# Kernel optimization log

Hardware: AMD Instinct MI355X
Metric: run time of the kernel (lower is better)

Reference implementation:

```python
import jax, jax.numpy as jnp
import numpy as np

T = 8  # num_temp_tokens (init arg)
K = 3  # routing conv kernel size (hardcoded in module)


def setup_inputs() -> dict:
    key = jax.random.key(0)
    ks = jax.random.split(key, 7)
    C, CO, NE = 384, 1152, 4
    BT, N = 256, 197
    s = 0.02
    return {
        "x": jax.random.normal(ks[0], (BT, N, C), dtype=jnp.float32),
        "rf_w": jax.random.normal(ks[1], (NE, C), dtype=jnp.float32) * s,
        "rf_b": jax.random.normal(ks[2], (NE,), dtype=jnp.float32) * s,
        "moe_w": jax.random.normal(ks[3], (NE, CO, C, K), dtype=jnp.float32) * s,
        "moe_b": jax.random.normal(ks[4], (NE, CO), dtype=jnp.float32) * s,
        "weight": jax.random.normal(ks[5], (CO, C), dtype=jnp.float32) * s,
        "bias": jax.random.normal(ks[6], (CO,), dtype=jnp.float32) * s,
    }


def _routing(cls, rf_w, rf_b, moe_w, moe_b):
    # cls: (b, C, T). route_func_linear_cls_token_moe forward.
    pooled = cls.mean(axis=2)                       # global avg pool over T -> (b, C)
    rf = pooled @ rf_w.T + rf_b                     # 1x1 conv -> (b, num_experts)
    w = jnp.einsum('be,eock->bock', rf, moe_w)      # per-sample mixed weights (b, 3C, C, K)
    br = rf @ moe_b                                 # per-sample mixed bias (b, 3C)
    clsp = jnp.pad(cls, ((0, 0), (0, 0), (K // 2, K // 2)))
    # sliding windows over T: (b, C, T, K)
    clsw = jnp.stack([clsp[:, :, k:k + cls.shape[2]] for k in range(K)], axis=-1)
    routing = jnp.einsum('bock,bctk->bot', w, clsw) + br[:, :, None] + 1.0  # (b, 3C, T)
    return routing


def reference(x, rf_w, rf_b, moe_w, moe_b, weight, bias):
    bt, n, C = x.shape
    b = bt // T
    xb = x.reshape(b, T, n, C)                      # '(b t) n c -> b t n c'
    cls = xb[:, :, 0, :].transpose(0, 2, 1)         # (b, C, T) cls token stream
    routing = _routing(cls, rf_w, rf_b, moe_w, moe_b)  # (b, 3C, T)
    r = routing.transpose(0, 2, 1)                  # (b, T, 3C)
    rq, rk, rv = jnp.split(r, 3, axis=-1)           # each (b, T, C)
    Wq, Wk, Wv = jnp.split(weight, 3, axis=0)       # each (C, C)
    bq, bk, bv = jnp.split(bias, 3)                 # each (C,)

    def branch(rr, Wc, bc):
        # grouped 1x1 conv with per-(b,t) cin-scaled weight:
        # out[b,t,o,n] = sum_c Wc[o,c] * rr[b,t,c] * x[b,t,n,c] + bc[o]*rr[b,t,o]
        xs = xb * rr[:, :, None, :]                 # (b, T, n, C)
        return jnp.einsum('btnc,oc->bton', xs, Wc) + (bc[None, None, :] * rr)[..., None]

    oq = branch(rq, Wq, bq)
    ok = branch(rk, Wk, bk)
    ov = branch(rv, Wv, bv)
    out = jnp.concatenate([oq, ok, ov], axis=2)     # (b, T, 3C, n)
    return out.reshape(bt, 3 * C, n)
```

## Files before the change

kernel.cpp:

```cpp
#include <hip/hip_runtime.h>
#include <hip/hip_bf16.h>

typedef __attribute__((ext_vector_type(8))) short short8;
typedef __attribute__((ext_vector_type(4))) short short4v;
typedef __attribute__((ext_vector_type(4))) float f32x4;

__device__ __forceinline__ short f2bf(float f) {
    union { float f; unsigned u; } v; v.f = f;
    unsigned r = v.u + 0x7FFF + ((v.u >> 16) & 1);
    return (short)(r >> 16);
}

__device__ __forceinline__ void gll16(const short* g, short* l) {
    __builtin_amdgcn_global_load_lds(
        (const __attribute__((address_space(1))) void*)g,
        (__attribute__((address_space(3))) void*)l, 16, 0, 0);
}

#define NE 4
#define CC 384
#define CO 1152
#define TT 8
#define NN 197
#define NPAD 224
#define NB 32
#define BT 256
#define MOEW_ELEMS 5308416
#define W_ELEMS    442368

__global__ __launch_bounds__(256) void prep_kernel(
    const float* __restrict__ x, const float* __restrict__ rf_w,
    const float* __restrict__ rf_b, const float* __restrict__ moe_w,
    const float* __restrict__ weight,
    short* __restrict__ moeWb, short* __restrict__ Wb,
    short* __restrict__ Yb, float* __restrict__ rf)
{
    int blk = blockIdx.x, tid = threadIdx.x;
    if (blk < NB) {
        __shared__ float clsL[TT * CC];
        __shared__ float pooled[CC];
        int b = blk;
        for (int flat = tid; flat < TT * CC; flat += 256) {
            int t = flat / CC, c = flat - t * CC;
            clsL[flat] = x[(size_t)(b * TT + t) * NN * CC + c];
        }
        __syncthreads();
        for (int c = tid; c < CC; c += 256) {
            float s = 0.f;
            #pragma unroll
            for (int t = 0; t < TT; t++) s += clsL[t * CC + c];
            pooled[c] = s * 0.125f;
        }
        for (int t = 0; t < TT; t++)
            for (int flat = tid; flat < CC * 3; flat += 256) {
                int c = flat / 3, k = flat - c * 3;
                int u = t + k - 1;
                float v = (u >= 0 && u < TT) ? clsL[u * CC + c] : 0.f;
                Yb[(size_t)(b * TT + t) * (CC * 3) + flat] = f2bf(v);
            }
        __syncthreads();
        int wave = tid >> 6, lane = tid & 63;
        float p = 0.f;
        for (int c = lane; c < CC; c += 64) p += pooled[c] * rf_w[wave * CC + c];
        #pragma unroll
        for (int off = 32; off; off >>= 1) p += __shfl_down(p, off, 64);
        if (lane == 0) rf[b * NE + wave] = p + rf_b[wave];
    } else {
        const long NU = (MOEW_ELEMS + W_ELEMS) / 4;
        long step = (long)(gridDim.x - NB) * 256;
        for (long unit = (long)(blk - NB) * 256 + tid; unit < NU; unit += step) {
            long idx = unit * 4;
            float4 v; short* dst;
            if (idx < MOEW_ELEMS) { v = *(const float4*)(moe_w + idx); dst = moeWb + idx; }
            else { long j = idx - MOEW_ELEMS; v = *(const float4*)(weight + j); dst = Wb + j; }
            short4v s;
            s.x = f2bf(v.x); s.y = f2bf(v.y); s.z = f2bf(v.z); s.w = f2bf(v.w);
            *(short4v*)dst = s;
        }
    }
}

__global__ __launch_bounds__(256) void gemm_P(
    const short* __restrict__ A, const short* __restrict__ B, float* __restrict__ P)
{
    __shared__ short A_lds[64 * 64];
    __shared__ short B_lds[64 * 64];
    int bm = blockIdx.x, bn = blockIdx.y, tid = threadIdx.x;
    int wave = tid >> 6, lane = tid & 63, l15 = lane & 15, lq = lane >> 4;
    f32x4 acc[4];
    #pragma unroll
    for (int j = 0; j < 4; j++) acc[j] = (f32x4){0.f, 0.f, 0.f, 0.f};

    for (int kk = 0; kk < 1152 / 64; kk++) {
        __syncthreads();
        #pragma unroll
        for (int j2 = 0; j2 < 2; j2++) {
            int flat = j2 * 256 + tid;
            int row = flat >> 3, seg = flat & 7;
            gll16(A + (size_t)(bm * 64 + row) * 1152 + kk * 64 + seg * 8, &A_lds[flat * 8]);
            gll16(B + (size_t)(bn * 64 + row) * 1152 + kk * 64 + seg * 8, &B_lds[flat * 8]);
        }
        __syncthreads();
        #pragma unroll
        for (int ks = 0; ks < 2; ks++) {
            short8 a = *(short8*)&A_lds[(wave * 16 + l15) * 64 + ks * 32 + lq * 8];
            #pragma unroll
            for (int j = 0; j < 4; j++) {
                short8 bfr = *(short8*)&B_lds[(j * 16 + l15) * 64 + ks * 32 + lq * 8];
                acc[j] = __builtin_amdgcn_mfma_f32_16x16x32_bf16(a, bfr, acc[j], 0, 0, 0);
            }
        }
    }
    #pragma unroll
    for (int j = 0; j < 4; j++)
        #pragma unroll
        for (int reg = 0; reg < 4; reg++) {
            int row = bm * 64 + wave * 16 + lq * 4 + reg;
            int col = bn * 64 + j * 16 + l15;
            P[(size_t)row * 256 + col] = acc[j][reg];
        }
}

__global__ __launch_bounds__(256) void combine_kernel(
    const float* __restrict__ P, const float* __restrict__ rf,
    const float* __restrict__ moe_b, float* __restrict__ r_ws)
{
    __shared__ float rf_l[NB * NE];
    int o = blockIdx.x, tid = threadIdx.x;
    if (tid < NB * NE) rf_l[tid] = rf[tid];
    __syncthreads();
    int b = tid >> 3;
    float acc = 1.0f;
    #pragma unroll
    for (int e = 0; e < NE; e++)
        acc += rf_l[b * NE + e] * (P[(size_t)(e * CO + o) * 256 + tid] + moe_b[e * CO + o]);
    r_ws[(size_t)tid * CO + o] = acc;
}

__global__ __launch_bounds__(256) void xs_scale(
    const float* __restrict__ x, const float* __restrict__ r_ws,
    short* __restrict__ xs)
{
    __shared__ float r_l[CO];
    int bt = blockIdx.x, ng = blockIdx.y, tid = threadIdx.x;
    for (int i = tid; i < CO; i += 256) r_l[i] = r_ws[(size_t)bt * CO + i];
    __syncthreads();
    #pragma unroll
    for (int it = 0; it < 6; it++) {
        int idx = it * 256 + tid;
        int row = idx / 96, cu = idx - row * 96;
        int n = ng * 16 + row;
        float4 v = {0.f, 0.f, 0.f, 0.f};
        if (n < NN) v = *(const float4*)(x + ((size_t)bt * NN + n) * CC + cu * 4);
        #pragma unroll
        for (int br = 0; br < 3; br++) {
            const float* rp = &r_l[br * CC + cu * 4];
            short4v s;
            s.x = f2bf(v.x * rp[0]);
            s.y = f2bf(v.y * rp[1]);
            s.z = f2bf(v.z * rp[2]);
            s.w = f2bf(v.w * rp[3]);
            *(short4v*)(xs + ((size_t)(bt * 3 + br) * NPAD + n) * CC + cu * 4) = s;
        }
    }
}

__global__ __launch_bounds__(256) void main_gemm(
    const short* __restrict__ xs, const short* __restrict__ Wb,
    const float* __restrict__ r_ws, const float* __restrict__ bias,
    float* __restrict__ out)
{
    __shared__ short A_lds[128 * 64];
    __shared__ short B_lds[112 * 64];

    int g = blockIdx.x;
    int u = g & 7, w2 = g >> 3;
    int mt = w2 % 9;
    int pq = u + 8 * (w2 / 9);
    int bt = pq >> 1, nt = pq & 1;
    int tid = threadIdx.x;
    int br = mt / 3;

    const short* Abase = Wb + (size_t)(mt * 128) * CC;
    const short* Bbase = xs + ((size_t)(bt * 3 + br) * NPAD + nt * 112) * CC;

    f32x4 acc[2][7];
    #pragma unroll
    for (int i = 0; i < 2; i++)
        #pragma unroll
        for (int j = 0; j < 7; j++) acc[i][j] = (f32x4){0.f, 0.f, 0.f, 0.f};

    int wave = tid >> 6, lane = tid & 63, l15 = lane & 15, lq = lane >> 4;
    int l7 = l15 & 7;

    for (int kk = 0; kk < CC / 64; kk++) {
        __syncthreads();
        #pragma unroll
        for (int j2 = 0; j2 < 4; j2++) {
            int flat = j2 * 256 + tid;
            int row = flat >> 3, ss = flat & 7;
            int seg = ss ^ (row & 7);
            gll16(Abase + (size_t)row * CC + kk * 64 + seg * 8, &A_lds[flat * 8]);
        }
        #pragma unroll
        for (int j2 = 0; j2 < 4; j2++) {
            int flat = j2 * 256 + tid;
            if (flat < 896) {
                int row = flat >> 3, ss = flat & 7;
                int seg = ss ^ (row & 7);
                gll16(Bbase + (size_t)row * CC + kk * 64 + seg * 8, &B_lds[flat * 8]);
            }
        }
        __syncthreads();
        #pragma unroll
        for (int ks = 0; ks < 2; ks++) {
            int sx = (ks * 4 + lq) ^ l7;
            short8 a0 = *(short8*)&A_lds[(wave * 32      + l15) * 64 + sx * 8];
            short8 a1 = *(short8*)&A_lds[(wave * 32 + 16 + l15) * 64 + sx * 8];
            #pragma unroll
            for (int j = 0; j < 7; j++) {
                short8 bfr = *(short8*)&B_lds[(j * 16 + l15) * 64 + sx * 8];
                acc[0][j] = __builtin_amdgcn_mfma_f32_16x16x32_bf16(a0, bfr, acc[0][j], 0, 0, 0);
                acc[1][j] = __builtin_amdgcn_mfma_f32_16x16x32_bf16(a1, bfr, acc[1][j], 0, 0, 0);
            }
        }
    }

    size_t outbase = (size_t)bt * (CO * NN);
    #pragma unroll
    for (int mi = 0; mi < 2; mi++)
        #pragma unroll
        for (int reg = 0; reg < 4; reg++) {
            int o = mt * 128 + wave * 32 + mi * 16 + lq * 4 + reg;
            float bo = bias[o] * r_ws[(size_t)bt * CO + o];
            #pragma unroll
            for (int j = 0; j < 7; j++) {
                int n = nt * 112 + j * 16 + l15;
                if (n < NN) out[outbase + (size_t)o * NN + n] = acc[mi][j][reg] + bo;
            }
        }
}

extern "C" void kernel_launch(void* const* d_in, const int* in_sizes, int n_in,
                              void* d_out, int out_size, void* d_ws, size_t ws_size,
                              hipStream_t stream) {
    const float* x      = (const float*)d_in[0];
    const float* rf_w   = (const float*)d_in[1];
    const float* rf_b   = (const float*)d_in[2];
    const float* moe_w  = (const float*)d_in[3];
    const float* moe_b  = (const float*)d_in[4];
    const float* weight = (const float*)d_in[5];
    const float* bias   = (const float*)d_in[6];
    float* out = (float*)d_out;

    char* ws = (char*)d_ws;
    short* Wb    = (short*)(ws + 0);
    short* moeWb = (short*)(ws + 884736);
    short* Yb    = (short*)(ws + 11501568);
    float* rf    = (float*)(ws + 12091392);
    float* P     = (float*)(ws + 12091904);
    float* r_ws  = (float*)(ws + 16810496);
    short* xs    = (short*)(ws + 17990144);

    prep_kernel<<<512, 256, 0, stream>>>(x, rf_w, rf_b, moe_w, weight, moeWb, Wb, Yb, rf);
    gemm_P<<<dim3(72, 4), 256, 0, stream>>>(moeWb, Yb, P);
    combine_kernel<<<1152, 256, 0, stream>>>(P, rf, moe_b, r_ws);
    xs_scale<<<dim3(256, 14), 256, 0, stream>>>(x, r_ws, xs);
    main_gemm<<<4608, 256, 0, stream>>>(xs, Wb, r_ws, bias, out);
}
```

Baseline: 466.6 us.

## Fuse routing-scaled bf16 conversion of x into main GEMM with double buffering

```diff
diff --git a/kernel.cpp b/kernel.cpp
--- a/kernel.cpp
+++ b/kernel.cpp
@@ -22,7 +22,6 @@
 #define CO 1152
 #define TT 8
 #define NN 197
-#define NPAD 224
 #define NB 32
 #define BT 256
 #define MOEW_ELEMS 5308416
@@ -137,41 +136,13 @@
     r_ws[(size_t)tid * CO + o] = acc;
 }
 
-__global__ __launch_bounds__(256) void xs_scale(
-    const float* __restrict__ x, const float* __restrict__ r_ws,
-    short* __restrict__ xs)
-{
-    __shared__ float r_l[CO];
-    int bt = blockIdx.x, ng = blockIdx.y, tid = threadIdx.x;
-    for (int i = tid; i < CO; i += 256) r_l[i] = r_ws[(size_t)bt * CO + i];
-    __syncthreads();
-    #pragma unroll
-    for (int it = 0; it < 6; it++) {
-        int idx = it * 256 + tid;
-        int row = idx / 96, cu = idx - row * 96;
-        int n = ng * 16 + row;
-        float4 v = {0.f, 0.f, 0.f, 0.f};
-        if (n < NN) v = *(const float4*)(x + ((size_t)bt * NN + n) * CC + cu * 4);
-        #pragma unroll
-        for (int br = 0; br < 3; br++) {
-            const float* rp = &r_l[br * CC + cu * 4];
-            short4v s;
-            s.x = f2bf(v.x * rp[0]);
-            s.y = f2bf(v.y * rp[1]);
-            s.z = f2bf(v.z * rp[2]);
-            s.w = f2bf(v.w * rp[3]);
-            *(short4v*)(xs + ((size_t)(bt * 3 + br) * NPAD + n) * CC + cu * 4) = s;
-        }
-    }
-}
-
-__global__ __launch_bounds__(256) void main_gemm(
-    const short* __restrict__ xs, const short* __restrict__ Wb,
+__global__ __launch_bounds__(256) void main_gemm_fused(
+    const float* __restrict__ x, const short* __restrict__ Wb,
     const float* __restrict__ r_ws, const float* __restrict__ bias,
     float* __restrict__ out)
 {
-    __shared__ short A_lds[128 * 64];
-    __shared__ short B_lds[112 * 64];
+    __shared__ short A_lds[2][128 * 64];
+    __shared__ short B_lds[2][112 * 64];
 
     int g = blockIdx.x;
     int u = g & 7, w2 = g >> 3;
@@ -182,44 +153,85 @@
     int br = mt / 3;
 
     const short* Abase = Wb + (size_t)(mt * 128) * CC;
-    const short* Bbase = xs + ((size_t)(bt * 3 + br) * NPAD + nt * 112) * CC;
-
-    f32x4 acc[2][7];
-    #pragma unroll
-    for (int i = 0; i < 2; i++)
-        #pragma unroll
-        for (int j = 0; j < 7; j++) acc[i][j] = (f32x4){0.f, 0.f, 0.f, 0.f};
 
     int wave = tid >> 6, lane = tid & 63, l15 = lane & 15, lq = lane >> 4;
     int l7 = l15 & 7;
-
-    for (int kk = 0; kk < CC / 64; kk++) {
-        __syncthreads();
+    int oct = tid & 7;
+    int rbase = tid >> 3;
+
+    const float* xbase = x + ((size_t)bt * NN + nt * 112) * CC + oct * 8;
+    const float* rbp   = r_ws + (size_t)bt * CO + br * CC + oct * 8;
+
+    f32x4 acc[2][7];
+    #pragma unroll
+    for (int i = 0; i < 2; i++)
+        #pragma unroll
+        for (int j = 0; j < 7; j++) acc[i][j] = (f32x4){0.f, 0.f, 0.f, 0.f};
+
+    float4 xr[8];
+    float4 rr0, rr1;
+
+    auto prefetch = [&](int t) {
+        rr0 = *(const float4*)(rbp + t * 64);
+        rr1 = *(const float4*)(rbp + t * 64 + 4);
+        #pragma unroll
+        for (int j2 = 0; j2 < 4; j2++) {
+            int row = j2 * 32 + rbase;
+            float4 z = {0.f, 0.f, 0.f, 0.f};
+            xr[2 * j2] = z; xr[2 * j2 + 1] = z;
+            if (row < 112 && nt * 112 + row < NN) {
+                const float* p = xbase + (size_t)row * CC + t * 64;
+                xr[2 * j2]     = *(const float4*)p;
+                xr[2 * j2 + 1] = *(const float4*)(p + 4);
+            }
+        }
+    };
+    auto issueA = [&](int t, int buf) {
         #pragma unroll
         for (int j2 = 0; j2 < 4; j2++) {
             int flat = j2 * 256 + tid;
             int row = flat >> 3, ss = flat & 7;
             int seg = ss ^ (row & 7);
-            gll16(Abase + (size_t)row * CC + kk * 64 + seg * 8, &A_lds[flat * 8]);
-        }
-        #pragma unroll
-        for (int j2 = 0; j2 < 4; j2++) {
-            int flat = j2 * 256 + tid;
-            if (flat < 896) {
-                int row = flat >> 3, ss = flat & 7;
-                int seg = ss ^ (row & 7);
-                gll16(Bbase + (size_t)row * CC + kk * 64 + seg * 8, &B_lds[flat * 8]);
-            }
-        }
-        __syncthreads();
+            gll16(Abase + (size_t)row * CC + t * 64 + seg * 8, &A_lds[buf][flat * 8]);
+        }
+    };
+
+    prefetch(0);
+    issueA(0, 0);
+
+    #pragma unroll
+    for (int t = 0; t < 6; t++) {
+        int pb = t & 1;
+        {
+            short* Bd = &B_lds[pb][0];
+            #pragma unroll
+            for (int j2 = 0; j2 < 4; j2++) {
+                int row = j2 * 32 + rbase;
+                if (j2 < 3 || rbase < 16) {
+                    int ss = oct ^ (row & 7);
+                    float4 a = xr[2 * j2], b = xr[2 * j2 + 1];
+                    short8 s;
+                    s[0] = f2bf(a.x * rr0.x); s[1] = f2bf(a.y * rr0.y);
+                    s[2] = f2bf(a.z * rr0.z); s[3] = f2bf(a.w * rr0.w);
+                    s[4] = f2bf(b.x * rr1.x); s[5] = f2bf(b.y * rr1.y);
+                    s[6] = f2bf(b.z * rr1.z); s[7] = f2bf(b.w * rr1.w);
+                    *(short8*)&Bd[row * 64 + ss * 8] = s;
+                }
+            }
+        }
+        __syncthreads();
+        if (t < 5) {
+            prefetch(t + 1);
+            issueA(t + 1, pb ^ 1);
+        }
         #pragma unroll
         for (int ks = 0; ks < 2; ks++) {
             int sx = (ks * 4 + lq) ^ l7;
-            short8 a0 = *(short8*)&A_lds[(wave * 32      + l15) * 64 + sx * 8];
-            short8 a1 = *(short8*)&A_lds[(wave * 32 + 16 + l15) * 64 + sx * 8];
+            short8 a0 = *(short8*)&A_lds[pb][(wave * 32      + l15) * 64 + sx * 8];
+            short8 a1 = *(short8*)&A_lds[pb][(wave * 32 + 16 + l15) * 64 + sx * 8];
             #pragma unroll
             for (int j = 0; j < 7; j++) {
-                short8 bfr = *(short8*)&B_lds[(j * 16 + l15) * 64 + sx * 8];
+                short8 bfr = *(short8*)&B_lds[pb][(j * 16 + l15) * 64 + sx * 8];
                 acc[0][j] = __builtin_amdgcn_mfma_f32_16x16x32_bf16(a0, bfr, acc[0][j], 0, 0, 0);
                 acc[1][j] = __builtin_amdgcn_mfma_f32_16x16x32_bf16(a1, bfr, acc[1][j], 0, 0, 0);
             }
@@ -260,11 +272,9 @@
     float* rf    = (float*)(ws + 12091392);
     float* P     = (float*)(ws + 12091904);
     float* r_ws  = (float*)(ws + 16810496);
-    short* xs    = (short*)(ws + 17990144);
 
     prep_kernel<<<512, 256, 0, stream>>>(x, rf_w, rf_b, moe_w, weight, moeWb, Wb, Yb, rf);
     gemm_P<<<dim3(72, 4), 256, 0, stream>>>(moeWb, Yb, P);
     combine_kernel<<<1152, 256, 0, stream>>>(P, rf, moe_b, r_ws);
-    xs_scale<<<dim3(256, 14), 256, 0, stream>>>(x, r_ws, xs);
-    main_gemm<<<4608, 256, 0, stream>>>(xs, Wb, r_ws, bias, out);
-}
+    main_gemm_fused<<<4608, 256, 0, stream>>>(x, Wb, r_ws, bias, out);
+}
```

After: 474.8 us. About the same (+1.8%).
